# Kernel tuning notes

Measured on AMD Instinct MI355X. Metric: run time of the kernel, lower is better.

The kernel has to match this reference:

```python
import jax, jax.numpy as jnp
import numpy as np

N = 100_000      # nodes
E = 1_600_000    # edges (avg degree 16)
D_IN = 256
D_OUT = 128


def setup_inputs() -> dict:
    key = jax.random.key(0)
    ks = jax.random.split(key, 13)
    stdv = 1.0 / np.sqrt(D_OUT)      # matches reset_parameters
    std_att = 1.0                    # att_vec_* have fan 1 -> stdv 1
    std_av = 1.0 / np.sqrt(3.0)
    return {
        "x": jax.random.normal(ks[0], (N, D_IN), dtype=jnp.float32),
        "edge_src": jax.random.randint(ks[1], (E,), 0, N),
        "edge_dst": jax.random.randint(ks[2], (E,), 0, N),
        "w_low": jax.random.uniform(ks[3], (E,), dtype=jnp.float32) / 16.0,   # ~normalized adj
        "w_high": jax.random.normal(ks[4], (E,), dtype=jnp.float32) / 16.0,    # high-pass weights can be +/-
        "w_unnorm": jax.random.uniform(ks[5], (E,), dtype=jnp.float32),
        "W_low": jax.random.uniform(ks[6], (D_IN, D_OUT), jnp.float32, -stdv, stdv),
        "W_high": jax.random.uniform(ks[7], (D_IN, D_OUT), jnp.float32, -stdv, stdv),
        "W_mlp": jax.random.uniform(ks[8], (D_IN, D_OUT), jnp.float32, -stdv, stdv),
        "a_low": jax.random.uniform(ks[9], (D_OUT, 1), jnp.float32, -std_att, std_att),
        "a_high": jax.random.uniform(ks[10], (D_OUT, 1), jnp.float32, -std_att, std_att),
        "a_mlp": jax.random.uniform(ks[11], (D_OUT, 1), jnp.float32, -std_att, std_att),
        "att_vec": jax.random.uniform(ks[12], (3, 3), jnp.float32, -std_av, std_av),
    }


def _spmm(w, src, dst, h, n):
    # sparse [n,n] @ dense [n,d]: gather source rows, weight, scatter-add to dest
    return jax.ops.segment_sum(w[:, None] * h[src], dst, num_segments=n)


def reference(x, edge_src, edge_dst, w_low, w_high, w_unnorm,
              W_low, W_high, W_mlp, a_low, a_high, a_mlp, att_vec):
    n = x.shape[0]
    # variant=False path: relu(spmm(adj, x @ W))
    h_low = jax.nn.relu(_spmm(w_low, edge_src, edge_dst, x @ W_low, n))
    h_high = jax.nn.relu(_spmm(w_high, edge_src, edge_dst, x @ W_high, n))
    h_mlp = jax.nn.relu(x @ W_mlp)
    # attention3: sigmoid of per-branch scalar scores -> 3x3 mix -> softmax (T=3)
    scores = jnp.concatenate([h_low @ a_low, h_high @ a_high, h_mlp @ a_mlp], axis=1)  # [n,3]
    att = jax.nn.softmax((jax.nn.sigmoid(scores) @ att_vec) / 3.0, axis=1)
    return 3.0 * (att[:, 0:1] * h_low + att[:, 1:2] * h_high + att[:, 2:3] * h_mlp)
```

## Files before the change

### kernel.cpp

```cpp
#include <hip/hip_runtime.h>
#include <hip/hip_bf16.h>
#include <math.h>

#define D_IN   256
#define D_OUT  128
#define NHB    256

typedef __attribute__((ext_vector_type(8))) short short8;
typedef __attribute__((ext_vector_type(4))) float floatx4;

__device__ __forceinline__ unsigned short f2bf(float f) {
  union { float f; unsigned u; } v; v.f = f;
  unsigned r = v.u + 0x7fffu + ((v.u >> 16) & 1u);
  return (unsigned short)(r >> 16);
}

__global__ __launch_bounds__(256) void hist_prep_kernel(
    const float* __restrict__ Wl, const float* __restrict__ Wh,
    const float* __restrict__ Wm, unsigned short* __restrict__ Bpack,
    const int* __restrict__ dst, int* __restrict__ bh, int E, int NB1) {
  __shared__ int hist[1024];
  const int bid = blockIdx.x;
  const int t = threadIdx.x;
  if (bid < NHB) {
    for (int k = t; k < NB1; k += 256) hist[k] = 0;
    __syncthreads();
    const int chunk = (E + NHB - 1) / NHB;
    const int base = bid * chunk;
    const int lim = min(E, base + chunk);
    for (int e = base + t; e < lim; e += 256) atomicAdd(&hist[dst[e] >> 7], 1);
    __syncthreads();
    for (int k = t; k < NB1; k += 256) bh[k * NHB + bid] = hist[k];
  } else {
    int tt = (bid - NHB) * 256 + t;
    int j = tt & 7;
    int lane = (tt >> 3) & 63;
    int f = tt >> 9;
    int nt = f % 24, kt = f / 24;
    int k = kt * 32 + (lane >> 4) * 8 + j;
    int n_ = nt * 16 + (lane & 15);
    const float* W = (n_ < 128) ? Wl : (n_ < 256 ? Wh : Wm);
    Bpack[tt] = f2bf(W[k * D_OUT + (n_ & 127)]);
  }
}

__global__ __launch_bounds__(256) void scan1_kernel(
    const int* __restrict__ cnt, int* __restrict__ outp,
    int* __restrict__ bsum, int n) {
  __shared__ int sd[256];
  int t = threadIdx.x;
  int base = blockIdx.x * 1024 + t * 4;
  int v0 = base + 0 < n ? cnt[base + 0] : 0;
  int v1 = base + 1 < n ? cnt[base + 1] : 0;
  int v2 = base + 2 < n ? cnt[base + 2] : 0;
  int v3 = base + 3 < n ? cnt[base + 3] : 0;
  int tsum = v0 + v1 + v2 + v3;
  sd[t] = tsum;
  __syncthreads();
  for (int off = 1; off < 256; off <<= 1) {
    int add = (t >= off) ? sd[t - off] : 0;
    __syncthreads();
    sd[t] += add;
    __syncthreads();
  }
  int excl = sd[t] - tsum;
  if (base + 0 < n) outp[base + 0] = excl;
  if (base + 1 < n) outp[base + 1] = excl + v0;
  if (base + 2 < n) outp[base + 2] = excl + v0 + v1;
  if (base + 3 < n) outp[base + 3] = excl + v0 + v1 + v2;
  if (t == 255) bsum[blockIdx.x] = sd[255];
}

__global__ __launch_bounds__(256) void scan2_kernel(int* __restrict__ bsum,
                                                    int nb) {
  __shared__ int sd[256];
  int t = threadIdx.x;
  int v = t < nb ? bsum[t] : 0;
  sd[t] = v;
  __syncthreads();
  for (int off = 1; off < 256; off <<= 1) {
    int add = (t >= off) ? sd[t - off] : 0;
    __syncthreads();
    sd[t] += add;
    __syncthreads();
  }
  if (t < nb) bsum[t] = sd[t] - v;
}

#define LDSROW 392
__global__ __launch_bounds__(512, 4) void gemm_sort_kernel(
    const float* __restrict__ x,
    const unsigned short* __restrict__ Bpack, unsigned short* __restrict__ Zg,
    unsigned short* __restrict__ Zm, int n_nodes, const int* __restrict__ src,
    const int* __restrict__ dst, const float* __restrict__ wlo,
    const float* __restrict__ whi, const int* __restrict__ bhscan,
    const int* __restrict__ bsum, uint2* __restrict__ tmp, int E, int NB1) {
  __shared__ unsigned short lds[16384];
  const int bid = blockIdx.x;

  int gemm_id;
  if (bid < 2 * NHB) {
    if ((bid & 1) == 0) {
      int rb = bid >> 1;
      int* cur = (int*)lds;
      int t = threadIdx.x;
      for (int k = t; k < NB1; k += 512) {
        int idx = k * NHB + rb;
        cur[k] = bhscan[idx] + bsum[idx >> 10];
      }
      __syncthreads();
      const int chunk = (E + NHB - 1) / NHB;
      const int base = rb * chunk;
      const int lim = min(E, base + chunk);
      for (int e = base + t; e < lim; e += 512) {
        int d = dst[e];
        int pos = atomicAdd(&cur[d >> 7], 1);
        unsigned wl = f2bf(wlo[e]), wh = f2bf(whi[e]);
        tmp[pos] = make_uint2((unsigned)src[e] | ((unsigned)(d & 127) << 20),
                              wl | (wh << 16));
      }
      return;
    }
    gemm_id = bid >> 1;
  } else {
    gemm_id = bid - 2 * NHB + NHB;
  }

  const int lane = threadIdx.x & 63;
  const int w = threadIdx.x >> 6;
  const int rowbase = gemm_id * 64;
  const int m16 = lane & 15, quad = lane >> 4;

  {
    const float4* xf = (const float4*)x;
#pragma unroll
    for (int i = 0; i < 4; i++) {
      int idx = i * 512 + threadIdx.x;
      int row = idx >> 5, c = idx & 31;
      int gr = rowbase + row;
      if (gr > n_nodes - 1) gr = n_nodes - 1;
      float4 f0 = xf[(size_t)gr * 64 + c * 2];
      float4 f1 = xf[(size_t)gr * 64 + c * 2 + 1];
      unsigned w0, w1, w2, w3;
      asm("v_cvt_pk_bf16_f32 %0, %1, %2" : "=v"(w0) : "v"(f0.x), "v"(f0.y));
      asm("v_cvt_pk_bf16_f32 %0, %1, %2" : "=v"(w1) : "v"(f0.z), "v"(f0.w));
      asm("v_cvt_pk_bf16_f32 %0, %1, %2" : "=v"(w2) : "v"(f1.x), "v"(f1.y));
      asm("v_cvt_pk_bf16_f32 %0, %1, %2" : "=v"(w3) : "v"(f1.z), "v"(f1.w));
      union { uint4 u; short8 s8; } cv;
      cv.u = make_uint4(w0, w1, w2, w3);
      int pc = (c & ~7) | ((c ^ row) & 7);
      ((short8*)lds)[row * 32 + pc] = cv.s8;
    }
  }
  __syncthreads();

  floatx4 acc[4][3];
#pragma unroll
  for (int s = 0; s < 4; s++)
#pragma unroll
    for (int c = 0; c < 3; c++) acc[s][c] = (floatx4)(0.f);

  const short8* bp = (const short8*)Bpack + lane;

#pragma unroll
  for (int kt = 0; kt < 8; kt++) {
    short8 a[4];
#pragma unroll
    for (int s = 0; s < 4; s++) {
      int r_ = s * 16 + m16;
      int c_ = kt * 4 + quad;
      int pc = (c_ & ~7) | ((c_ ^ r_) & 7);
      a[s] = ((const short8*)lds)[r_ * 32 + pc];
    }
#pragma unroll
    for (int c = 0; c < 3; c++) {
      short8 b = bp[(kt * 24 + w * 3 + c) * 64];
#pragma unroll
      for (int s = 0; s < 4; s++)
        acc[s][c] =
            __builtin_amdgcn_mfma_f32_16x16x32_bf16(a[s], b, acc[s][c], 0, 0, 0);
    }
  }

  __syncthreads();
  unsigned short* tile = lds;

#pragma unroll
  for (int half = 0; half < 2; half++) {
    if (half) __syncthreads();
#pragma unroll
    for (int s = 0; s < 2; s++)
#pragma unroll
      for (int c = 0; c < 3; c++)
#pragma unroll
        for (int r = 0; r < 4; r++)
          tile[(s * 16 + quad * 4 + r) * LDSROW + (w * 3 + c) * 16 + m16] =
              f2bf(acc[half * 2 + s][c][r]);
    __syncthreads();
#pragma unroll
    for (int it = 0; it < 3; it++) {
      int chunk = it * 512 + threadIdx.x;
      int row = chunk / 48, c8 = chunk % 48;
      int grow = rowbase + half * 32 + row;
      if (grow < n_nodes) {
        short8 v = *(const short8*)&tile[row * LDSROW + c8 * 8];
        if (c8 < 32)
          *(short8*)(Zg + (size_t)grow * 256 + c8 * 8) = v;
        else
          *(short8*)(Zm + (size_t)grow * 128 + (c8 - 32) * 8) = v;
      }
    }
  }
}

__global__ __launch_bounds__(256) void fine_kernel(
    const uint2* __restrict__ tmp, const int* __restrict__ bhscan,
    const int* __restrict__ bsum, uint2* __restrict__ meta,
    int* __restrict__ rowptr, int NB1, int n, int E) {
  __shared__ int fh[128];
  __shared__ int sd[128];
  __shared__ int cur[128];
  const int b = blockIdx.x;
  const int t = threadIdx.x;
  auto scanidx = [&](int i) { return bhscan[i] + bsum[i >> 10]; };
  const int s0 = scanidx(b * NHB);
  const int s1 = (b == NB1 - 1) ? E : scanidx((b + 1) * NHB);

  if (t < 128) fh[t] = 0;
  __syncthreads();
  for (int i = s0 + t; i < s1; i += 256)
    atomicAdd(&fh[(tmp[i].x >> 20) & 127], 1);
  __syncthreads();

  if (t < 128) sd[t] = fh[t];
  __syncthreads();
  for (int off = 1; off < 128; off <<= 1) {
    int add = (t >= off && t < 128) ? sd[t - off] : 0;
    __syncthreads();
    if (t < 128) sd[t] += add;
    __syncthreads();
  }
  if (t < 128) {
    int excl = sd[t] - fh[t];
    cur[t] = excl;
    int node = b * 128 + t;
    if (node < n) rowptr[node] = s0 + excl;
  }
  if (b == 0 && t == 0) rowptr[n] = E;
  __syncthreads();

  for (int i = s0 + t; i < s1; i += 256) {
    uint2 v = tmp[i];
    int d = (v.x >> 20) & 127;
    int pos = s0 + atomicAdd(&cur[d], 1);
    meta[pos] = make_uint2(v.x & 0xFFFFFu, v.y);
  }
}

__global__ __launch_bounds__(128) void node_kernel(
    const unsigned short* __restrict__ Zg, const unsigned short* __restrict__ Zm,
    const int* __restrict__ rowptr, const unsigned long long* __restrict__ meta,
    const float* __restrict__ a_low, const float* __restrict__ a_high,
    const float* __restrict__ a_mlp, const float* __restrict__ att_vec,
    float* __restrict__ out, int n_nodes) {
  int node = blockIdx.x * 2 + (threadIdx.x >> 6);
  if (node >= n_nodes) return;
  node = __builtin_amdgcn_readfirstlane(node);
  const int lane = threadIdx.x & 63;
  const int isHigh = lane >> 5;
  const int dbase = (lane & 31) * 4;
  const char* Zb = (const char*)Zg;

  const int start = rowptr[node];
  const int end = rowptr[node + 1];

  float acc0 = 0.f, acc1 = 0.f, acc2 = 0.f, acc3 = 0.f;
  auto wsel = [&](unsigned p) {
    return __uint_as_float(isHigh ? (p & 0xffff0000u) : (p << 16));
  };
  auto step = [&](uint2 z, float wv) {
    acc0 += wv * __uint_as_float(z.x << 16);
    acc1 += wv * __uint_as_float(z.x & 0xffff0000u);
    acc2 += wv * __uint_as_float(z.y << 16);
    acc3 += wv * __uint_as_float(z.y & 0xffff0000u);
  };

  int j = start;
  const int nfull = (end - start) & ~7;
  for (; j < start + nfull; j += 8) {
    unsigned long long m[8];
    uint2 z[8];
#pragma unroll
    for (int u = 0; u < 8; u++) m[u] = __builtin_nontemporal_load(&meta[j + u]);
#pragma unroll
    for (int u = 0; u < 8; u++)
      z[u] = *(const uint2*)(Zb + ((size_t)(unsigned)m[u]) * 512 + lane * 8);
#pragma unroll
    for (int u = 0; u < 8; u++) step(z[u], wsel((unsigned)(m[u] >> 32)));
  }
  for (; j < end; j++) {
    unsigned long long m0 = __builtin_nontemporal_load(&meta[j]);
    uint2 z0 = *(const uint2*)(Zb + ((size_t)(unsigned)m0) * 512 + lane * 8);
    step(z0, wsel((unsigned)(m0 >> 32)));
  }

  float h0 = fmaxf(acc0, 0.f), h1 = fmaxf(acc1, 0.f);
  float h2 = fmaxf(acc2, 0.f), h3 = fmaxf(acc3, 0.f);

  unsigned long long zmq = __builtin_nontemporal_load(
      (const unsigned long long*)((const char*)Zm + (size_t)node * 256 +
                                  (size_t)(lane & 31) * 8));
  unsigned zmx = (unsigned)zmq, zmy = (unsigned)(zmq >> 32);
  float q0 = fmaxf(__uint_as_float(zmx << 16), 0.f);
  float q1 = fmaxf(__uint_as_float(zmx & 0xffff0000u), 0.f);
  float q2 = fmaxf(__uint_as_float(zmy << 16), 0.f);
  float q3 = fmaxf(__uint_as_float(zmy & 0xffff0000u), 0.f);

  const float* av_b = isHigh ? a_high : a_low;
  float4 ab = *(const float4*)&av_b[dbase];
  float4 am = *(const float4*)&a_mlp[dbase];
  float v1 = h0 * ab.x + h1 * ab.y + h2 * ab.z + h3 * ab.w;
  float v2 = isHigh ? 0.f : (q0 * am.x + q1 * am.y + q2 * am.z + q3 * am.w);
#pragma unroll
  for (int off = 1; off < 32; off <<= 1) {
    v1 += __shfl_xor(v1, off);
    v2 += __shfl_xor(v2, off);
  }
  float s_lo = __shfl(v1, 0);
  float s_hi = __shfl(v1, 32);
  float s_ml = __shfl(v2, 0);

  float g0 = 1.f / (1.f + __expf(-s_lo));
  float g1 = 1.f / (1.f + __expf(-s_hi));
  float g2 = 1.f / (1.f + __expf(-s_ml));
  const float inv3 = 1.f / 3.f;
  float m0 = (g0 * att_vec[0] + g1 * att_vec[3] + g2 * att_vec[6]) * inv3;
  float m1 = (g0 * att_vec[1] + g1 * att_vec[4] + g2 * att_vec[7]) * inv3;
  float m2 = (g0 * att_vec[2] + g1 * att_vec[5] + g2 * att_vec[8]) * inv3;
  float mx = fmaxf(m0, fmaxf(m1, m2));
  float e0 = __expf(m0 - mx), e1 = __expf(m1 - mx), e2 = __expf(m2 - mx);
  float inv = 1.f / (e0 + e1 + e2);
  float c0 = 3.f * inv * e0, c1 = 3.f * inv * e1, c2 = 3.f * inv * e2;

  float hh0 = __shfl_xor(h0, 32);
  float hh1 = __shfl_xor(h1, 32);
  float hh2 = __shfl_xor(h2, 32);
  float hh3 = __shfl_xor(h3, 32);

  if (!isHigh) {
    floatx4 o;
    o.x = c0 * h0 + c1 * hh0 + c2 * q0;
    o.y = c0 * h1 + c1 * hh1 + c2 * q1;
    o.z = c0 * h2 + c1 * hh2 + c2 * q2;
    o.w = c0 * h3 + c1 * hh3 + c2 * q3;
    __builtin_nontemporal_store(o,
                                (floatx4*)&out[(size_t)node * D_OUT + dbase]);
  }
}

extern "C" void kernel_launch(void* const* d_in, const int* in_sizes, int n_in,
                              void* d_out, int out_size, void* d_ws,
                              size_t ws_size, hipStream_t stream) {
  const float* x    = (const float*)d_in[0];
  const int*   esrc = (const int*)d_in[1];
  const int*   edst = (const int*)d_in[2];
  const float* wlo  = (const float*)d_in[3];
  const float* whi  = (const float*)d_in[4];
  const float* Wl   = (const float*)d_in[6];
  const float* Wh   = (const float*)d_in[7];
  const float* Wm   = (const float*)d_in[8];
  const float* alo  = (const float*)d_in[9];
  const float* ahi  = (const float*)d_in[10];
  const float* amlp = (const float*)d_in[11];
  const float* av   = (const float*)d_in[12];
  float* out = (float*)d_out;

  const int N = in_sizes[0] / D_IN;
  const int E = in_sizes[1];
  const int NB1 = (N + 127) >> 7;
  const int M = NB1 * NHB;

  char* ws = (char*)d_ws;
  size_t off = 0;
  auto carve = [&](size_t bytes) -> void* {
    void* p = ws + off;
    off = (off + bytes + 255) & ~(size_t)255;
    return p;
  };
  unsigned short* Zg     = (unsigned short*)carve((size_t)N * 256 * 2);
  unsigned short* Zm     = (unsigned short*)carve((size_t)N * 128 * 2);
  unsigned short* Bpack  = (unsigned short*)carve(98304 * 2);
  int*   bh     = (int*)carve((size_t)M * 4);
  int*   bhscan = (int*)carve((size_t)M * 4);
  int*   bsum   = (int*)carve(256 * 4);
  int*   rowptr = (int*)carve((size_t)(N + 1) * 4);
  uint2* tmp    = (uint2*)carve((size_t)E * 8);
  uint2* meta   = (uint2*)carve((size_t)E * 8);

  hist_prep_kernel<<<NHB + 384, 256, 0, stream>>>(Wl, Wh, Wm, Bpack, edst, bh,
                                                  E, NB1);
  int nb1s = (M + 1023) / 1024;
  scan1_kernel<<<nb1s, 256, 0, stream>>>(bh, bhscan, bsum, M);
  scan2_kernel<<<1, 256, 0, stream>>>(bsum, nb1s);

  int ngemm = (N + 63) / 64;
  gemm_sort_kernel<<<ngemm + NHB, 512, 0, stream>>>(
      x, Bpack, Zg, Zm, N, esrc, edst, wlo, whi, bhscan, bsum, tmp, E, NB1);

  fine_kernel<<<NB1, 256, 0, stream>>>(tmp, bhscan, bsum, meta, rowptr, NB1, N,
                                       E);

  node_kernel<<<(N + 1) / 2, 128, 0, stream>>>(
      Zg, Zm, rowptr, (const unsigned long long*)meta, alo, ahi, amlp, av, out,
      N);
}
```

Before: 395.8 us.

## Spread GEMM tiles across scan, scatter and fine-sort kernels to overlap

The standalone GEMM work is split into four chunks, each co-launched with one of the serial CSR-building stages (scan1, scan2, scatter, fine bucket sort) inside a shared kernel. Blocks of the two roles are interleaved. The goal is to hide the latency-bound, low-occupancy scan and sort stages behind useful matmul work and to remove idle GPU time between launches. The scan block size doubles to 512 threads, so the bsum indexing changes to >>11. The cost is 512-thread blocks with fixed LDS for the small stages and hand-tuned chunk sizes (120/60/1000/rest).

Result: slower. 413.4 us (+4.4%).

```diff
diff --git a/kernel.cpp b/kernel.cpp
--- a/kernel.cpp
+++ b/kernel.cpp
@@ -44,88 +44,11 @@
   }
 }
 
-__global__ __launch_bounds__(256) void scan1_kernel(
-    const int* __restrict__ cnt, int* __restrict__ outp,
-    int* __restrict__ bsum, int n) {
-  __shared__ int sd[256];
-  int t = threadIdx.x;
-  int base = blockIdx.x * 1024 + t * 4;
-  int v0 = base + 0 < n ? cnt[base + 0] : 0;
-  int v1 = base + 1 < n ? cnt[base + 1] : 0;
-  int v2 = base + 2 < n ? cnt[base + 2] : 0;
-  int v3 = base + 3 < n ? cnt[base + 3] : 0;
-  int tsum = v0 + v1 + v2 + v3;
-  sd[t] = tsum;
-  __syncthreads();
-  for (int off = 1; off < 256; off <<= 1) {
-    int add = (t >= off) ? sd[t - off] : 0;
-    __syncthreads();
-    sd[t] += add;
-    __syncthreads();
-  }
-  int excl = sd[t] - tsum;
-  if (base + 0 < n) outp[base + 0] = excl;
-  if (base + 1 < n) outp[base + 1] = excl + v0;
-  if (base + 2 < n) outp[base + 2] = excl + v0 + v1;
-  if (base + 3 < n) outp[base + 3] = excl + v0 + v1 + v2;
-  if (t == 255) bsum[blockIdx.x] = sd[255];
-}
-
-__global__ __launch_bounds__(256) void scan2_kernel(int* __restrict__ bsum,
-                                                    int nb) {
-  __shared__ int sd[256];
-  int t = threadIdx.x;
-  int v = t < nb ? bsum[t] : 0;
-  sd[t] = v;
-  __syncthreads();
-  for (int off = 1; off < 256; off <<= 1) {
-    int add = (t >= off) ? sd[t - off] : 0;
-    __syncthreads();
-    sd[t] += add;
-    __syncthreads();
-  }
-  if (t < nb) bsum[t] = sd[t] - v;
-}
-
 #define LDSROW 392
-__global__ __launch_bounds__(512, 4) void gemm_sort_kernel(
-    const float* __restrict__ x,
+__device__ __forceinline__ void gemm_tile(
+    int gemm_id, unsigned short* lds, const float* __restrict__ x,
     const unsigned short* __restrict__ Bpack, unsigned short* __restrict__ Zg,
-    unsigned short* __restrict__ Zm, int n_nodes, const int* __restrict__ src,
-    const int* __restrict__ dst, const float* __restrict__ wlo,
-    const float* __restrict__ whi, const int* __restrict__ bhscan,
-    const int* __restrict__ bsum, uint2* __restrict__ tmp, int E, int NB1) {
-  __shared__ unsigned short lds[16384];
-  const int bid = blockIdx.x;
-
-  int gemm_id;
-  if (bid < 2 * NHB) {
-    if ((bid & 1) == 0) {
-      int rb = bid >> 1;
-      int* cur = (int*)lds;
-      int t = threadIdx.x;
-      for (int k = t; k < NB1; k += 512) {
-        int idx = k * NHB + rb;
-        cur[k] = bhscan[idx] + bsum[idx >> 10];
-      }
-      __syncthreads();
-      const int chunk = (E + NHB - 1) / NHB;
-      const int base = rb * chunk;
-      const int lim = min(E, base + chunk);
-      for (int e = base + t; e < lim; e += 512) {
-        int d = dst[e];
-        int pos = atomicAdd(&cur[d >> 7], 1);
-        unsigned wl = f2bf(wlo[e]), wh = f2bf(whi[e]);
-        tmp[pos] = make_uint2((unsigned)src[e] | ((unsigned)(d & 127) << 20),
-                              wl | (wh << 16));
-      }
-      return;
-    }
-    gemm_id = bid >> 1;
-  } else {
-    gemm_id = bid - 2 * NHB + NHB;
-  }
-
+    unsigned short* __restrict__ Zm, int n_nodes) {
   const int lane = threadIdx.x & 63;
   const int w = threadIdx.x >> 6;
   const int rowbase = gemm_id * 64;
@@ -213,22 +136,166 @@
   }
 }
 
-__global__ __launch_bounds__(256) void fine_kernel(
+__device__ __forceinline__ void scan1_block(int sb, const int* __restrict__ bh,
+                                            int* __restrict__ bhscan,
+                                            int* __restrict__ bsum, int M,
+                                            int* sd) {
+  int t = threadIdx.x;
+  int base = sb * 2048 + t * 4;
+  int v0 = base + 0 < M ? bh[base + 0] : 0;
+  int v1 = base + 1 < M ? bh[base + 1] : 0;
+  int v2 = base + 2 < M ? bh[base + 2] : 0;
+  int v3 = base + 3 < M ? bh[base + 3] : 0;
+  int tsum = v0 + v1 + v2 + v3;
+  sd[t] = tsum;
+  __syncthreads();
+  for (int off = 1; off < 512; off <<= 1) {
+    int add = (t >= off) ? sd[t - off] : 0;
+    __syncthreads();
+    sd[t] += add;
+    __syncthreads();
+  }
+  int excl = sd[t] - tsum;
+  if (base + 0 < M) bhscan[base + 0] = excl;
+  if (base + 1 < M) bhscan[base + 1] = excl + v0;
+  if (base + 2 < M) bhscan[base + 2] = excl + v0 + v1;
+  if (base + 3 < M) bhscan[base + 3] = excl + v0 + v1 + v2;
+  if (t == 511) bsum[sb] = sd[511];
+}
+
+__global__ __launch_bounds__(512, 4) void scan1_gemm_kernel(
+    const int* __restrict__ bh, int* __restrict__ bhscan,
+    int* __restrict__ bsum, int M, int nscan, int ngA, int gbase,
+    const float* __restrict__ x, const unsigned short* __restrict__ Bpack,
+    unsigned short* __restrict__ Zg, unsigned short* __restrict__ Zm,
+    int n_nodes) {
+  __shared__ unsigned short lds[16384];
+  const int bid = blockIdx.x;
+  const int mn = min(nscan, ngA), m2 = 2 * mn;
+  int role, idx;
+  if (bid < m2) {
+    role = bid & 1;
+    idx = bid >> 1;
+  } else if (nscan < ngA) {
+    role = 1;
+    idx = bid - m2 + mn;
+  } else {
+    role = 0;
+    idx = bid - m2 + mn;
+  }
+  if (role == 0)
+    scan1_block(idx, bh, bhscan, bsum, M, (int*)lds);
+  else
+    gemm_tile(gbase + idx, lds, x, Bpack, Zg, Zm, n_nodes);
+}
+
+__global__ __launch_bounds__(512, 4) void scan2_gemm_kernel(
+    int* __restrict__ bsum, int nb, int gbase, const float* __restrict__ x,
+    const unsigned short* __restrict__ Bpack, unsigned short* __restrict__ Zg,
+    unsigned short* __restrict__ Zm, int n_nodes) {
+  __shared__ unsigned short lds[16384];
+  const int bid = blockIdx.x;
+  if (bid == 0) {
+    int* sd = (int*)lds;
+    int t = threadIdx.x;
+    int v = t < nb ? bsum[t] : 0;
+    sd[t] = v;
+    __syncthreads();
+    for (int off = 1; off < 512; off <<= 1) {
+      int add = (t >= off) ? sd[t - off] : 0;
+      __syncthreads();
+      sd[t] += add;
+      __syncthreads();
+    }
+    if (t < nb) bsum[t] = sd[t] - v;
+  } else {
+    gemm_tile(gbase + bid - 1, lds, x, Bpack, Zg, Zm, n_nodes);
+  }
+}
+
+__global__ __launch_bounds__(512, 4) void scatter_gemm_kernel(
+    const int* __restrict__ src, const int* __restrict__ dst,
+    const float* __restrict__ wlo, const float* __restrict__ whi,
+    const int* __restrict__ bhscan, const int* __restrict__ bsum,
+    uint2* __restrict__ tmp, int E, int NB1, int ngC, int gbase,
+    const float* __restrict__ x, const unsigned short* __restrict__ Bpack,
+    unsigned short* __restrict__ Zg, unsigned short* __restrict__ Zm,
+    int n_nodes) {
+  __shared__ unsigned short lds[16384];
+  const int bid = blockIdx.x;
+  const int mn = min(NHB, ngC), m2 = 2 * mn;
+  int role, idx;
+  if (bid < m2) {
+    role = bid & 1;
+    idx = bid >> 1;
+  } else if (NHB < ngC) {
+    role = 1;
+    idx = bid - m2 + mn;
+  } else {
+    role = 0;
+    idx = bid - m2 + mn;
+  }
+  if (role == 0) {
+    int rb = idx;
+    int* cur = (int*)lds;
+    int t = threadIdx.x;
+    for (int k = t; k < NB1; k += 512) {
+      int i2 = k * NHB + rb;
+      cur[k] = bhscan[i2] + bsum[i2 >> 11];
+    }
+    __syncthreads();
+    const int chunk = (E + NHB - 1) / NHB;
+    const int base = rb * chunk;
+    const int lim = min(E, base + chunk);
+    for (int e = base + t; e < lim; e += 512) {
+      int d = dst[e];
+      int pos = atomicAdd(&cur[d >> 7], 1);
+      unsigned wl = f2bf(wlo[e]), wh = f2bf(whi[e]);
+      tmp[pos] = make_uint2((unsigned)src[e] | ((unsigned)(d & 127) << 20),
+                            wl | (wh << 16));
+    }
+  } else {
+    gemm_tile(gbase + idx, lds, x, Bpack, Zg, Zm, n_nodes);
+  }
+}
+
+__global__ __launch_bounds__(512, 4) void fine_gemm_kernel(
     const uint2* __restrict__ tmp, const int* __restrict__ bhscan,
     const int* __restrict__ bsum, uint2* __restrict__ meta,
-    int* __restrict__ rowptr, int NB1, int n, int E) {
-  __shared__ int fh[128];
-  __shared__ int sd[128];
-  __shared__ int cur[128];
-  const int b = blockIdx.x;
+    int* __restrict__ rowptr, int NB1, int n, int E, int ngD, int gbase,
+    const float* __restrict__ x, const unsigned short* __restrict__ Bpack,
+    unsigned short* __restrict__ Zg, unsigned short* __restrict__ Zm,
+    int n_nodes) {
+  __shared__ unsigned short lds[16384];
+  const int bid = blockIdx.x;
+  const int mn = min(NB1, ngD), m2 = 2 * mn;
+  int role, idx;
+  if (bid < m2) {
+    role = bid & 1;
+    idx = bid >> 1;
+  } else if (NB1 < ngD) {
+    role = 1;
+    idx = bid - m2 + mn;
+  } else {
+    role = 0;
+    idx = bid - m2 + mn;
+  }
+  if (role == 1) {
+    gemm_tile(gbase + idx, lds, x, Bpack, Zg, Zm, n_nodes);
+    return;
+  }
+  const int b = idx;
+  int* fh = (int*)lds;
+  int* sd = fh + 128;
+  int* cur = fh + 256;
   const int t = threadIdx.x;
-  auto scanidx = [&](int i) { return bhscan[i] + bsum[i >> 10]; };
+  auto scanidx = [&](int i) { return bhscan[i] + bsum[i >> 11]; };
   const int s0 = scanidx(b * NHB);
   const int s1 = (b == NB1 - 1) ? E : scanidx((b + 1) * NHB);
 
   if (t < 128) fh[t] = 0;
   __syncthreads();
-  for (int i = s0 + t; i < s1; i += 256)
+  for (int i = s0 + t; i < s1; i += 512)
     atomicAdd(&fh[(tmp[i].x >> 20) & 127], 1);
   __syncthreads();
 
@@ -249,7 +316,7 @@
   if (b == 0 && t == 0) rowptr[n] = E;
   __syncthreads();
 
-  for (int i = s0 + t; i < s1; i += 256) {
+  for (int i = s0 + t; i < s1; i += 512) {
     uint2 v = tmp[i];
     int d = (v.x >> 20) & 127;
     int pos = s0 + atomicAdd(&cur[d], 1);
@@ -392,24 +459,30 @@
   unsigned short* Bpack  = (unsigned short*)carve(98304 * 2);
   int*   bh     = (int*)carve((size_t)M * 4);
   int*   bhscan = (int*)carve((size_t)M * 4);
-  int*   bsum   = (int*)carve(256 * 4);
+  int*   bsum   = (int*)carve(512 * 4);
   int*   rowptr = (int*)carve((size_t)(N + 1) * 4);
   uint2* tmp    = (uint2*)carve((size_t)E * 8);
   uint2* meta   = (uint2*)carve((size_t)E * 8);
 
+  int ngemm = (N + 63) / 64;
+  int NGA = min(ngemm, 120);
+  int NGB = min(ngemm - NGA, 60);
+  int NGC = min(ngemm - NGA - NGB, 1000);
+  int NGD = ngemm - NGA - NGB - NGC;
+  int nscan = (M + 2047) / 2048;
+
   hist_prep_kernel<<<NHB + 384, 256, 0, stream>>>(Wl, Wh, Wm, Bpack, edst, bh,
                                                   E, NB1);
-  int nb1s = (M + 1023) / 1024;
-  scan1_kernel<<<nb1s, 256, 0, stream>>>(bh, bhscan, bsum, M);
-  scan2_kernel<<<1, 256, 0, stream>>>(bsum, nb1s);
-
-  int ngemm = (N + 63) / 64;
-  gemm_sort_kernel<<<ngemm + NHB, 512, 0, stream>>>(
-      x, Bpack, Zg, Zm, N, esrc, edst, wlo, whi, bhscan, bsum, tmp, E, NB1);
-
-  fine_kernel<<<NB1, 256, 0, stream>>>(tmp, bhscan, bsum, meta, rowptr, NB1, N,
-                                       E);
-
+  scan1_gemm_kernel<<<nscan + NGA, 512, 0, stream>>>(
+      bh, bhscan, bsum, M, nscan, NGA, 0, x, Bpack, Zg, Zm, N);
+  scan2_gemm_kernel<<<1 + NGB, 512, 0, stream>>>(bsum, nscan, NGA, x, Bpack,
+                                                 Zg, Zm, N);
+  scatter_gemm_kernel<<<NHB + NGC, 512, 0, stream>>>(
+      esrc, edst, wlo, whi, bhscan, bsum, tmp, E, NB1, NGC, NGA + NGB, x,
+      Bpack, Zg, Zm, N);
+  fine_gemm_kernel<<<NB1 + NGD, 512, 0, stream>>>(
+      tmp, bhscan, bsum, meta, rowptr, NB1, N, E, NGD, NGA + NGB + NGC, x,
+      Bpack, Zg, Zm, N);
   node_kernel<<<(N + 1) / 2, 128, 0, stream>>>(
       Zg, Zm, rowptr, (const unsigned long long*)meta, alo, ahi, amlp, av, out,
       N);
```
